# Kernel optimization log

Measured on AMD Instinct MI355X. Metric: run time of the kernel, lower is better.

## Reference

```python
import jax, jax.numpy as jnp
import numpy as np
from jax import lax

C = 256
R = 16
B, H, W = 8, 128, 128
TIME_STEPS = 3


def _dct_filter(C):
    # Matches HCFDA._get_dct_filter exactly (vectorized).
    k = np.arange(C)[:, None].astype(np.float64)
    l = np.arange(C)[None, :].astype(np.float64)
    term1 = np.cos((2 * k + 1) * l * np.pi / (2 * C))
    term2 = np.cos((2 * l + 1) * k * np.pi / (2 * C))
    d = (2.0 / C) * term1 * term2
    d[0, :] = np.sqrt(2.0) / C  # k==0 branch (cos term is 1)
    d[:, 0] = np.sqrt(2.0) / C  # l==0 branch (cos term is 1)
    d[0, 0] = 1.0 / C
    return d.astype(np.float32)


def setup_inputs() -> dict:
    key = jax.random.key(0)
    ks = jax.random.split(key, 5)
    x = jax.random.normal(ks[0], (B, C, H, W), dtype=jnp.float32)
    dct_w = jnp.asarray(_dct_filter(C))  # [C, C], frozen (requires_grad=False)
    # SE FC params (kaiming fan_out init, zero bias)
    w1 = jax.random.normal(ks[1], (C // R, C), dtype=jnp.float32) * np.sqrt(2.0 / (C // R))
    b1 = jnp.zeros((C // R,), dtype=jnp.float32)
    w2 = jax.random.normal(ks[2], (C, C // R), dtype=jnp.float32) * np.sqrt(2.0 / C)
    b2 = jnp.zeros((C,), dtype=jnp.float32)
    alpha = jnp.float32(0.1)
    lap = jnp.array([[0.05, 0.2, 0.05], [0.2, -1.0, 0.2], [0.05, 0.2, 0.05]], dtype=jnp.float32)
    return {"x": x, "dct_w": dct_w, "w1": w1, "b1": b1, "w2": w2, "b2": b2, "alpha": alpha, "lap": lap}


def reference(x, dct_w, w1, b1, w2, b2, alpha, lap):
    # 1x1 DCT conv: [B,C,H,W] x [Cout,Cin] -> [B,Cout,H,W]
    x_dct = jnp.einsum('bchw,oc->bohw', x, dct_w)
    temp = jnp.mean(x_dct, axis=1, keepdims=True)  # [B,1,H,W]
    kernel = lap.reshape(1, 1, 3, 3)
    for _ in range(TIME_STEPS):
        padded = jnp.pad(temp, ((0, 0), (0, 0), (1, 1), (1, 1)), mode='reflect')
        lapl = lax.conv_general_dilated(padded, kernel, window_strides=(1, 1), padding='VALID',
                                        dimension_numbers=('NCHW', 'OIHW', 'NCHW'))
        temp = temp + alpha * lapl
    heat_map = jax.nn.sigmoid(temp)  # [B,1,H,W]

    y_avg = jnp.mean(x, axis=(2, 3))  # [B,C]
    y_max = jnp.max(x, axis=(2, 3))   # [B,C]
    fc = lambda y: jax.nn.sigmoid(jax.nn.relu(y @ w1.T + b1) @ w2.T + b2)
    channel_att = (fc(y_avg) + fc(y_max))[:, :, None, None]  # [B,C,1,1]
    attention = jax.nn.sigmoid(channel_att * heat_map)       # [B,C,H,W]
    return x * attention
```

## Files before the change

kernel.cpp:

```cpp
#include <hip/hip_runtime.h>
#include <math.h>

#define C_ 256
#define R_ 16
#define B_ 8
#define H_ 128
#define W_ 128
#define HW_ (H_ * W_)
#define CG_ 8
#define CPG_ (C_ / CG_)
#define NCHUNK_ 16

typedef float f4_ __attribute__((ext_vector_type(4)));

__device__ __forceinline__ float sigmoidf_(float z) {
    return 1.0f / (1.0f + __expf(-z));
}

__device__ __forceinline__ int reflect_(int g) {
    if (g < 0) g = -g;
    if (g > 127) g = 254 - g;
    return g;
}

__global__ void k1_stats_temp(const float* __restrict__ x, const float* __restrict__ dct_w,
                              float* __restrict__ ptemp,
                              float* __restrict__ psum, float* __restrict__ pmax) {
    __shared__ float sm_[CPG_];
    __shared__ float pmred[8][CPG_];
    __shared__ float lsum[16][CPG_ + 1];
    __shared__ float lmax[16][CPG_ + 1];
    int tid = threadIdx.x;
    int bid = blockIdx.x;
    int b = bid >> 7, chunk = (bid >> 3) & 15, cg = bid & 7;

    {
        int c_l = tid & 31, oc = tid >> 5;
        const float* p = dct_w + cg * CPG_ + c_l;
        float pm = 0.0f;
        for (int k = 0; k < 32; ++k) pm += p[(oc * 32 + k) * C_];
        pmred[oc][c_l] = pm;
    }
    __syncthreads();
    if (tid < CPG_) {
        float t = 0.0f;
        for (int o = 0; o < 8; ++o) t += pmred[o][tid];
        sm_[tid] = t * (1.0f / C_);
    }
    __syncthreads();

    int pix = chunk * 1024 + tid * 4;
    const f4_* px = (const f4_*)(x + (size_t)(b * C_ + cg * CPG_) * HW_ + pix);
    int lane = tid & 63, wid = tid >> 6;
    int grp = (wid << 2) | (lane >> 4);
    bool writer = (lane & 15) == 0;

    f4_ acc = {0.0f, 0.0f, 0.0f, 0.0f};
#pragma unroll 2
    for (int c = 0; c < CPG_; ++c) {
        f4_ v = px[(size_t)c * (HW_ / 4)];
        float w = sm_[c];
        acc.x = fmaf(w, v.x, acc.x);
        acc.y = fmaf(w, v.y, acc.y);
        acc.z = fmaf(w, v.z, acc.z);
        acc.w = fmaf(w, v.w, acc.w);
        float s = (v.x + v.y) + (v.z + v.w);
        float mx = fmaxf(fmaxf(v.x, v.y), fmaxf(v.z, v.w));
        for (int mo = 8; mo >= 1; mo >>= 1) {
            s += __shfl_xor(s, mo, 16);
            mx = fmaxf(mx, __shfl_xor(mx, mo, 16));
        }
        if (writer) { lsum[grp][c] = s; lmax[grp][c] = mx; }
    }
    *(f4_*)(ptemp + (size_t)(cg * B_ + b) * HW_ + pix) = acc;
    __syncthreads();

    if (tid < CPG_) {
        float S = 0.0f, M = -3.402823466e+38f;
        for (int g = 0; g < 16; ++g) {
            S += lsum[g][tid];
            M = fmaxf(M, lmax[g][tid]);
        }
        psum[(size_t)(b * NCHUNK_ + chunk) * C_ + cg * CPG_ + tid] = S;
        pmax[(size_t)(b * NCHUNK_ + chunk) * C_ + cg * CPG_ + tid] = M;
    }
}

#define TS_ 38
__global__ void k2_heat_fc(const float* __restrict__ ptemp,
                           const float* __restrict__ psum, const float* __restrict__ pmax,
                           const float* __restrict__ w1, const float* __restrict__ b1,
                           const float* __restrict__ w2, const float* __restrict__ b2,
                           const float* __restrict__ alphap, const float* __restrict__ lapp,
                           float* __restrict__ heat, float* __restrict__ att) {
    int tid = threadIdx.x;
    if (blockIdx.x < 128) {
        __shared__ float sA[TS_ * TS_], sB[TS_ * TS_];
        int b = blockIdx.x >> 4;
        int tile = blockIdx.x & 15;
        int tr = (tile >> 2) * 32, tc = (tile & 3) * 32;
        for (int i = tid; i < TS_ * TS_; i += 256) {
            int lh = i / TS_, lw = i % TS_;
            int gh = reflect_(tr + lh - 3);
            int gw = reflect_(tc + lw - 3);
            size_t a = (size_t)gh * W_ + gw + (size_t)b * HW_;
            float v = 0.0f;
            for (int cg = 0; cg < CG_; ++cg) v += ptemp[(size_t)cg * B_ * HW_ + a];
            sA[i] = v;
        }
        float alpha = *alphap;
        float l0 = lapp[0], l1 = lapp[1], l2 = lapp[2],
              l3 = lapp[3], l4 = lapp[4], l5 = lapp[5],
              l6 = lapp[6], l7 = lapp[7], l8 = lapp[8];
        __syncthreads();
#define DIFF(src, lh, lw)                                                              \
        fmaf(alpha,                                                                    \
             l0 * src[(lh - 1) * TS_ + lw - 1] + l1 * src[(lh - 1) * TS_ + lw] +       \
             l2 * src[(lh - 1) * TS_ + lw + 1] + l3 * src[lh * TS_ + lw - 1] +         \
             l4 * src[lh * TS_ + lw] + l5 * src[lh * TS_ + lw + 1] +                   \
             l6 * src[(lh + 1) * TS_ + lw - 1] + l7 * src[(lh + 1) * TS_ + lw] +       \
             l8 * src[(lh + 1) * TS_ + lw + 1],                                        \
             src[lh * TS_ + lw])
        for (int i = tid; i < 36 * 36; i += 256) {
            int lh = i / 36 + 1, lw = i % 36 + 1;
            sB[lh * TS_ + lw] = DIFF(sA, lh, lw);
        }
        __syncthreads();
        for (int i = tid; i < 34 * 34; i += 256) {
            int lh = i / 34 + 2, lw = i % 34 + 2;
            sA[lh * TS_ + lw] = DIFF(sB, lh, lw);
        }
        __syncthreads();
        float* hb = heat + b * HW_;
        for (int i = tid; i < 32 * 32; i += 256) {
            int lh = i / 32 + 3, lw = i % 32 + 3;
            float v = DIFF(sA, lh, lw);
            hb[(tr + lh - 3) * W_ + (tc + lw - 3)] = sigmoidf_(v);
        }
#undef DIFF
    } else {
        __shared__ float sa[C_], sx[C_], ha[R_], hm[R_];
        int b = blockIdx.x - 128;
        float S = 0.0f, M = -3.402823466e+38f;
        for (int ch = 0; ch < NCHUNK_; ++ch) {
            S += psum[(size_t)(b * NCHUNK_ + ch) * C_ + tid];
            M = fmaxf(M, pmax[(size_t)(b * NCHUNK_ + ch) * C_ + tid]);
        }
        sa[tid] = S * (1.0f / HW_);
        sx[tid] = M;
        __syncthreads();
        if (tid < 2 * R_) {
            int j = tid & (R_ - 1);
            bool isMax = tid >= R_;
            const float* y = isMax ? sx : sa;
            float s = b1[j];
            for (int c = 0; c < C_; ++c) s = fmaf(w1[j * C_ + c], y[c], s);
            s = fmaxf(s, 0.0f);
            (isMax ? hm : ha)[j] = s;
        }
        __syncthreads();
        float s1 = b2[tid], s2 = s1;
        for (int j = 0; j < R_; ++j) {
            float w = w2[tid * R_ + j];
            s1 = fmaf(w, ha[j], s1);
            s2 = fmaf(w, hm[j], s2);
        }
        att[b * C_ + tid] = sigmoidf_(s1) + sigmoidf_(s2);
    }
}

__global__ void k3_out(const float* __restrict__ x, const float* __restrict__ att,
                       const float* __restrict__ heat, float* __restrict__ out) {
    int bid = blockIdx.x;
    int bc = bid >> 1, half = bid & 1;
    int b = bc >> 8;
    float a = att[bc];
    size_t base = (size_t)bc * HW_ + half * (HW_ / 2);
    const f4_* px = (const f4_*)(x + base);
    const f4_* ph = (const f4_*)(heat + b * HW_ + half * (HW_ / 2));
    f4_* po = (f4_*)(out + base);
    for (int i = threadIdx.x; i < HW_ / 8; i += 256) {
        f4_ v = px[i];
        f4_ h = ph[i];
        f4_ r;
        r.x = v.x * sigmoidf_(a * h.x);
        r.y = v.y * sigmoidf_(a * h.y);
        r.z = v.z * sigmoidf_(a * h.z);
        r.w = v.w * sigmoidf_(a * h.w);
        __builtin_nontemporal_store(r, &po[i]);
    }
}

extern "C" void kernel_launch(void* const* d_in, const int* in_sizes, int n_in,
                              void* d_out, int out_size, void* d_ws, size_t ws_size,
                              hipStream_t stream) {
    const float* x     = (const float*)d_in[0];
    const float* dct_w = (const float*)d_in[1];
    const float* w1    = (const float*)d_in[2];
    const float* b1    = (const float*)d_in[3];
    const float* w2    = (const float*)d_in[4];
    const float* b2    = (const float*)d_in[5];
    const float* alpha = (const float*)d_in[6];
    const float* lap   = (const float*)d_in[7];
    float* out = (float*)d_out;

    float* ws    = (float*)d_ws;
    float* psum  = ws;
    float* pmax  = ws + 32768;
    float* att   = ws + 65536;
    float* heat  = ws + 69632;
    float* ptemp = ws + 200704;

    k1_stats_temp<<<1024, 256, 0, stream>>>(x, dct_w, ptemp, psum, pmax);
    k2_heat_fc<<<136, 256, 0, stream>>>(ptemp, psum, pmax, w1, b1, w2, b2, alpha, lap, heat, att);
    k3_out<<<4096, 256, 0, stream>>>(x, att, heat, out);
}
```

Measured before the change: 75.62 us.

## Fuse heat diffusion, channel FC and output scaling into one per-row kernel

Merges the separate heat-map/FC kernel and the output kernel into one kernel with a block per (batch,row). Each block recomputes the 3-step stencil on a 7-row halo, redoes the channel FC per block, and then scales x across all channels for its row. This removes a kernel launch and the heat/att round trip through global memory, and lets the tiny 136-block stage run at full occupancy. In exchange the FC and halo stencil are recomputed redundantly in 1024 blocks, and x reads become strided per row (512-byte segments per channel). The k1 unroll factor also rises from 2 to 4.

```diff
diff --git a/kernel.cpp b/kernel.cpp
--- a/kernel.cpp
+++ b/kernel.cpp
@@ -56,7 +56,7 @@
     bool writer = (lane & 15) == 0;
 
     f4_ acc = {0.0f, 0.0f, 0.0f, 0.0f};
-#pragma unroll 2
+#pragma unroll 4
     for (int c = 0; c < CPG_; ++c) {
         f4_ v = px[(size_t)c * (HW_ / 4)];
         float w = sm_[c];
@@ -86,108 +86,112 @@
     }
 }
 
-#define TS_ 38
-__global__ void k2_heat_fc(const float* __restrict__ ptemp,
-                           const float* __restrict__ psum, const float* __restrict__ pmax,
-                           const float* __restrict__ w1, const float* __restrict__ b1,
-                           const float* __restrict__ w2, const float* __restrict__ b2,
-                           const float* __restrict__ alphap, const float* __restrict__ lapp,
-                           float* __restrict__ heat, float* __restrict__ att) {
+__global__ void __launch_bounds__(256)
+k2_fused(const float* __restrict__ x, const float* __restrict__ ptemp,
+         const float* __restrict__ psum, const float* __restrict__ pmax,
+         const float* __restrict__ w1, const float* __restrict__ b1,
+         const float* __restrict__ w2, const float* __restrict__ b2,
+         const float* __restrict__ alphap, const float* __restrict__ lapp,
+         float* __restrict__ out) {
+    __shared__ float sA[7 * W_];
+    __shared__ float sB[5 * W_];
+    __shared__ float hrow[W_];
+    __shared__ float att_s[C_], savg[C_], smax_[C_], ha[R_], hm[R_];
     int tid = threadIdx.x;
-    if (blockIdx.x < 128) {
-        __shared__ float sA[TS_ * TS_], sB[TS_ * TS_];
-        int b = blockIdx.x >> 4;
-        int tile = blockIdx.x & 15;
-        int tr = (tile >> 2) * 32, tc = (tile & 3) * 32;
-        for (int i = tid; i < TS_ * TS_; i += 256) {
-            int lh = i / TS_, lw = i % TS_;
-            int gh = reflect_(tr + lh - 3);
-            int gw = reflect_(tc + lw - 3);
-            size_t a = (size_t)gh * W_ + gw + (size_t)b * HW_;
-            float v = 0.0f;
-            for (int cg = 0; cg < CG_; ++cg) v += ptemp[(size_t)cg * B_ * HW_ + a];
-            sA[i] = v;
-        }
-        float alpha = *alphap;
-        float l0 = lapp[0], l1 = lapp[1], l2 = lapp[2],
-              l3 = lapp[3], l4 = lapp[4], l5 = lapp[5],
-              l6 = lapp[6], l7 = lapp[7], l8 = lapp[8];
-        __syncthreads();
-#define DIFF(src, lh, lw)                                                              \
-        fmaf(alpha,                                                                    \
-             l0 * src[(lh - 1) * TS_ + lw - 1] + l1 * src[(lh - 1) * TS_ + lw] +       \
-             l2 * src[(lh - 1) * TS_ + lw + 1] + l3 * src[lh * TS_ + lw - 1] +         \
-             l4 * src[lh * TS_ + lw] + l5 * src[lh * TS_ + lw + 1] +                   \
-             l6 * src[(lh + 1) * TS_ + lw - 1] + l7 * src[(lh + 1) * TS_ + lw] +       \
-             l8 * src[(lh + 1) * TS_ + lw + 1],                                        \
-             src[lh * TS_ + lw])
-        for (int i = tid; i < 36 * 36; i += 256) {
-            int lh = i / 36 + 1, lw = i % 36 + 1;
-            sB[lh * TS_ + lw] = DIFF(sA, lh, lw);
-        }
-        __syncthreads();
-        for (int i = tid; i < 34 * 34; i += 256) {
-            int lh = i / 34 + 2, lw = i % 34 + 2;
-            sA[lh * TS_ + lw] = DIFF(sB, lh, lw);
-        }
-        __syncthreads();
-        float* hb = heat + b * HW_;
-        for (int i = tid; i < 32 * 32; i += 256) {
-            int lh = i / 32 + 3, lw = i % 32 + 3;
-            float v = DIFF(sA, lh, lw);
-            hb[(tr + lh - 3) * W_ + (tc + lw - 3)] = sigmoidf_(v);
-        }
-#undef DIFF
-    } else {
-        __shared__ float sa[C_], sx[C_], ha[R_], hm[R_];
-        int b = blockIdx.x - 128;
+    int b = blockIdx.x >> 7, r = blockIdx.x & 127;
+
+    for (int i = tid; i < 7 * W_; i += 256) {
+        int lr = i >> 7, col = i & 127;
+        int gr = reflect_(r - 3 + lr);
+        size_t a = (size_t)b * HW_ + gr * W_ + col;
+        float v = 0.0f;
+#pragma unroll
+        for (int cg = 0; cg < CG_; ++cg) v += ptemp[(size_t)cg * (B_ * HW_) + a];
+        sA[i] = v;
+    }
+    {
         float S = 0.0f, M = -3.402823466e+38f;
         for (int ch = 0; ch < NCHUNK_; ++ch) {
             S += psum[(size_t)(b * NCHUNK_ + ch) * C_ + tid];
             M = fmaxf(M, pmax[(size_t)(b * NCHUNK_ + ch) * C_ + tid]);
         }
-        sa[tid] = S * (1.0f / HW_);
-        sx[tid] = M;
-        __syncthreads();
-        if (tid < 2 * R_) {
-            int j = tid & (R_ - 1);
-            bool isMax = tid >= R_;
-            const float* y = isMax ? sx : sa;
-            float s = b1[j];
-            for (int c = 0; c < C_; ++c) s = fmaf(w1[j * C_ + c], y[c], s);
-            s = fmaxf(s, 0.0f);
-            (isMax ? hm : ha)[j] = s;
-        }
-        __syncthreads();
+        savg[tid] = S * (1.0f / HW_);
+        smax_[tid] = M;
+    }
+    float alpha = *alphap;
+    float l0 = lapp[0], l1 = lapp[1], l2 = lapp[2],
+          l3 = lapp[3], l4 = lapp[4], l5 = lapp[5],
+          l6 = lapp[6], l7 = lapp[7], l8 = lapp[8];
+    __syncthreads();
+
+#define DIFF(src, lr, col, cm, cp)                                                     \
+    fmaf(alpha,                                                                        \
+         l0 * src[(lr - 1) * W_ + cm] + l1 * src[(lr - 1) * W_ + col] +                \
+         l2 * src[(lr - 1) * W_ + cp] + l3 * src[lr * W_ + cm] +                       \
+         l4 * src[lr * W_ + col] + l5 * src[lr * W_ + cp] +                            \
+         l6 * src[(lr + 1) * W_ + cm] + l7 * src[(lr + 1) * W_ + col] +                \
+         l8 * src[(lr + 1) * W_ + cp],                                                 \
+         src[lr * W_ + col])
+
+    for (int i = tid; i < 5 * W_; i += 256) {
+        int lr = (i >> 7) + 1, col = i & 127;
+        int cm = col ? col - 1 : 1;
+        int cp = (col < 127) ? col + 1 : 126;
+        sB[(lr - 1) * W_ + col] = DIFF(sA, lr, col, cm, cp);
+    }
+    __syncthreads();
+    for (int i = tid; i < 3 * W_; i += 256) {
+        int lr = (i >> 7) + 1, col = i & 127;
+        int cm = col ? col - 1 : 1;
+        int cp = (col < 127) ? col + 1 : 126;
+        sA[(lr - 1) * W_ + col] = DIFF(sB, lr, col, cm, cp);
+    }
+    __syncthreads();
+    if (tid < W_) {
+        int col = tid;
+        int cm = col ? col - 1 : 1;
+        int cp = (col < 127) ? col + 1 : 126;
+        hrow[col] = sigmoidf_(DIFF(sA, 1, col, cm, cp));
+    }
+#undef DIFF
+
+    if (tid < 2 * R_) {
+        int j = tid & (R_ - 1);
+        bool isMax = tid >= R_;
+        const float* y = isMax ? smax_ : savg;
+        float s = b1[j];
+        for (int c = 0; c < C_; ++c) s = fmaf(w1[j * C_ + c], y[c], s);
+        s = fmaxf(s, 0.0f);
+        (isMax ? hm : ha)[j] = s;
+    }
+    __syncthreads();
+    {
         float s1 = b2[tid], s2 = s1;
         for (int j = 0; j < R_; ++j) {
             float w = w2[tid * R_ + j];
             s1 = fmaf(w, ha[j], s1);
             s2 = fmaf(w, hm[j], s2);
         }
-        att[b * C_ + tid] = sigmoidf_(s1) + sigmoidf_(s2);
-    }
-}
-
-__global__ void k3_out(const float* __restrict__ x, const float* __restrict__ att,
-                       const float* __restrict__ heat, float* __restrict__ out) {
-    int bid = blockIdx.x;
-    int bc = bid >> 1, half = bid & 1;
-    int b = bc >> 8;
-    float a = att[bc];
-    size_t base = (size_t)bc * HW_ + half * (HW_ / 2);
-    const f4_* px = (const f4_*)(x + base);
-    const f4_* ph = (const f4_*)(heat + b * HW_ + half * (HW_ / 2));
-    f4_* po = (f4_*)(out + base);
-    for (int i = threadIdx.x; i < HW_ / 8; i += 256) {
-        f4_ v = px[i];
-        f4_ h = ph[i];
-        f4_ r;
-        r.x = v.x * sigmoidf_(a * h.x);
-        r.y = v.y * sigmoidf_(a * h.y);
-        r.z = v.z * sigmoidf_(a * h.z);
-        r.w = v.w * sigmoidf_(a * h.w);
-        __builtin_nontemporal_store(r, &po[i]);
+        att_s[tid] = sigmoidf_(s1) + sigmoidf_(s2);
+    }
+    __syncthreads();
+
+    size_t xbase = (size_t)b * C_ * HW_ + (size_t)r * W_;
+    int c0 = tid >> 5, col4 = tid & 31;
+    const f4_* hp = (const f4_*)hrow;
+    f4_ h = hp[col4];
+#pragma unroll 4
+    for (int cb = 0; cb < 32; ++cb) {
+        int c = cb * 8 + c0;
+        size_t off = xbase + (size_t)c * HW_ + col4 * 4;
+        f4_ v = *(const f4_*)(x + off);
+        float a = att_s[c];
+        f4_ o;
+        o.x = v.x * sigmoidf_(a * h.x);
+        o.y = v.y * sigmoidf_(a * h.y);
+        o.z = v.z * sigmoidf_(a * h.z);
+        o.w = v.w * sigmoidf_(a * h.w);
+        __builtin_nontemporal_store(o, (f4_*)(out + off));
     }
 }
 
@@ -207,11 +211,9 @@
     float* ws    = (float*)d_ws;
     float* psum  = ws;
     float* pmax  = ws + 32768;
-    float* att   = ws + 65536;
-    float* heat  = ws + 69632;
-    float* ptemp = ws + 200704;
+    float* ptemp = ws + 65536;
 
     k1_stats_temp<<<1024, 256, 0, stream>>>(x, dct_w, ptemp, psum, pmax);
-    k2_heat_fc<<<136, 256, 0, stream>>>(ptemp, psum, pmax, w1, b1, w2, b2, alpha, lap, heat, att);
-    k3_out<<<4096, 256, 0, stream>>>(x, att, heat, out);
-}
+    k2_fused<<<1024, 256, 0, stream>>>(x, ptemp, psum, pmax, w1, b1, w2, b2,
+                                       alpha, lap, out);
+}
```

Result: slower. 79.03 us (+4.5%).
